# Kernel optimization log

Measured on AMD Instinct MI355X. Metric: run time of the kernel, lower is better.

The kernel has to match this reference:

```python
import jax, jax.numpy as jnp
import numpy as np

N_INP = 128
N_HID = 512
N_OUT = 256
N_HEADS = 64
N_SM = 4
EPS_GN = 1e-5
TINY = 1e-14


def setup_inputs() -> dict:
    key = jax.random.key(0)
    ks = jax.random.split(key, 8)
    s = 0.05  # small init scale keeps softplus/softmax in a sane range
    f32 = jnp.float32
    return {
        "x": jax.random.normal(ks[0], (N_INP, N_INP), f32),
        "last_out_sm": jax.random.uniform(ks[1], (N_OUT, N_HEADS), f32),
        # grouped-conv weights, stored per-head with conv singleton dims squeezed
        "qw": jax.random.normal(ks[2], (N_HEADS, N_INP), f32) * s,            # Conv2d q
        "w1": jax.random.normal(ks[3], (N_HEADS, N_HID, N_INP), f32) * s,     # Conv1d l1
        "gn1_g": jnp.ones((N_HEADS, N_HID), f32),                             # GroupNorm ln_l1
        "gn1_b": jnp.zeros((N_HEADS, N_HID), f32),
        "w2": jax.random.normal(ks[4], (N_SM, N_HEADS, N_OUT, N_HID), f32) * s,  # Conv1d l2_n
        "gn2_g": jnp.ones((N_SM, N_HEADS, N_OUT), f32),                       # GroupNorm ln_l2_n
        "gn2_b": jnp.zeros((N_SM, N_HEADS, N_OUT), f32),
        "ws": jax.random.normal(ks[5], (N_HEADS, N_OUT, N_OUT), f32) * s,     # Conv1d scalar
        "woo": jax.random.normal(ks[6], (N_HEADS, 2 * N_OUT), f32) * s,       # Conv1d on_off
    }


def _group_norm(z, g, b):
    # normalize over the last (per-head channel) axis, biased variance, then affine
    mu = z.mean(-1, keepdims=True)
    var = z.var(-1, keepdims=True)
    return (z - mu) * jax.lax.rsqrt(var + EPS_GN) * g + b


def reference(x, last_out_sm, qw, w1, gn1_g, gn1_b, w2, gn2_g, gn2_b, ws, woo):
    n_out = last_out_sm.shape[0]
    # q: grouped Conv2d with kernel (1, n_inp) on replicated x -> per-head x @ qw_h
    sub = jnp.einsum("rc,hc->hr", x, qw)                     # (H, n_inp)
    # l1 (grouped 1x1 conv == per-head matmul) + GroupNorm(n_heads groups) + softplus
    h1 = jax.nn.softplus(_group_norm(jnp.einsum("hoi,hi->ho", w1, sub), gn1_g, gn1_b))  # (H, n_hid)
    # l2_n branches: per-head matmul + GroupNorm + softmax over n_out, summed over n_sm
    z = _group_norm(jnp.einsum("shoi,hi->sho", w2, h1), gn2_g, gn2_b)  # (S, H, n_out)
    out_sm = jax.nn.softmax(z, axis=-1).sum(0).T             # (n_out, H)
    # scalar branch: grouped 1x1 conv applied to ones -> row-sum of per-head weight
    scalar = ws.sum(-1).T                                    # (n_out, H)
    # on_off gate: per-head dot of [prod(last_out_sm, dim1), out_sm[:, h]] with woo_h
    last_prod = jnp.prod(last_out_sm, axis=1)                # (n_out,)
    gate_logit = woo[:, :n_out] @ last_prod + jnp.einsum("ho,oh->h", woo[:, n_out:], out_sm)
    on_off = jax.nn.sigmoid(gate_logit)                      # (H,)
    on_off_out_sm = on_off[None, :] * out_sm                 # (n_out, H)
    out_scaled = on_off_out_sm * scalar
    out_scaled = jnp.where(jnp.abs(out_scaled) <= TINY, TINY, out_scaled)
    return (jnp.clip(on_off_out_sm, TINY, None), out_scaled)
```

## Files before the change

### kernel.cpp

```cpp
#include <hip/hip_runtime.h>
#include <math.h>

#define N_INP 128
#define N_HID 512
#define N_OUT 256
#define N_HEADS 64
#define N_SM 4
#define EPS_GN 1e-5f
#define TINY 1e-14f

__device__ __forceinline__ float wave_sum(float v) {
#pragma unroll
  for (int off = 32; off; off >>= 1) v += __shfl_down(v, off);
  return v;
}

__device__ __forceinline__ float block_sum(float v, float* red) {
  int wave = threadIdx.x >> 6, lane = threadIdx.x & 63;
  int nw = blockDim.x >> 6;
  v = wave_sum(v);
  __syncthreads();
  if (lane == 0) red[wave] = v;
  __syncthreads();
  float s = 0.f;
  for (int i = 0; i < nw; ++i) s += red[i];
  return s;
}

__global__ __launch_bounds__(512) void k_z1(
    const float* __restrict__ x, const float* __restrict__ qw,
    const float* __restrict__ w1, float* __restrict__ z1,
    float* __restrict__ zstat) {
  int blk = blockIdx.x;
  int h = blk >> 2, oq = blk & 3;
  int tid = threadIdx.x, wave = tid >> 6, lane = tid & 63;
  __shared__ float sub_s[N_INP];
  __shared__ float2 wred[8];

  float2 qv = ((const float2*)(qw + h * N_INP))[lane];
  for (int r = wave; r < N_INP; r += 8) {
    float2 xv = ((const float2*)(x + r * N_INP))[lane];
    float p = wave_sum(xv.x * qv.x + xv.y * qv.y);
    if (lane == 0) sub_s[r] = p;
  }
  __syncthreads();

  float2 sv = ((const float2*)sub_s)[lane];
  const float* w1h = w1 + ((size_t)h * N_HID + (size_t)oq * 128) * N_INP;
  float zs = 0.f, zq = 0.f;
  for (int k = 0; k < 16; ++k) {
    int o = wave * 16 + k;
    float2 wv = ((const float2*)(w1h + (size_t)o * N_INP))[lane];
    float p = wave_sum(wv.x * sv.x + wv.y * sv.y);
    if (lane == 0) { z1[h * N_HID + oq * 128 + o] = p; zs += p; zq += p * p; }
  }
  if (lane == 0) wred[wave] = make_float2(zs, zq);
  __syncthreads();
  if (tid == 0) {
    float a = 0.f, b = 0.f;
    for (int i = 0; i < 8; ++i) { a += wred[i].x; b += wred[i].y; }
    zstat[blk * 2] = a;
    zstat[blk * 2 + 1] = b;
  }
}

__global__ __launch_bounds__(1024) void k_l2(
    const float* __restrict__ z1, const float* __restrict__ zstat,
    const float* __restrict__ g1, const float* __restrict__ b1,
    const float* __restrict__ w2, const float* __restrict__ g2,
    const float* __restrict__ b2, const float* __restrict__ wsc,
    float* __restrict__ part, float* __restrict__ scal) {
  int blk = blockIdx.x;
  int s = blk >> 6, h = blk & 63;
  int tid = threadIdx.x, wave = tid >> 6, lane = tid & 63;
  __shared__ float h1_s[N_HID];
  __shared__ float z_s[N_OUT];
  __shared__ float2 red2[16];
  __shared__ float red[16];

  const float* w2base = w2 + (size_t)blk * N_OUT * N_HID;
  const float4* row0 = (const float4*)(w2base + (size_t)(wave * 16) * N_HID);
  float4 wa = row0[lane];
  float4 wb = row0[64 + lane];

  float zsum = 0.f, zsq = 0.f;
#pragma unroll
  for (int q = 0; q < 4; ++q) {
    zsum += zstat[(h * 4 + q) * 2];
    zsq  += zstat[(h * 4 + q) * 2 + 1];
  }
  float mu1 = zsum * (1.f / N_HID);
  float var1 = zsq * (1.f / N_HID) - mu1 * mu1;
  float r1 = rsqrtf(var1 + EPS_GN);
  if (tid < N_HID) {
    float v1 = z1[h * N_HID + tid];
    float zz = (v1 - mu1) * r1 * g1[h * N_HID + tid] + b1[h * N_HID + tid];
    h1_s[tid] = fmaxf(zz, 0.f) + log1pf(expf(-fabsf(zz)));
  }
  __syncthreads();

  float4 ha = ((const float4*)h1_s)[lane];
  float4 hb = ((const float4*)h1_s)[64 + lane];

  for (int k = 0; k < 4; ++k) {
    int o = s * 64 + wave * 4 + k;
    float4 v = ((const float4*)(wsc + ((size_t)(h * N_OUT + o)) * N_OUT))[lane];
    float p = wave_sum(v.x + v.y + v.z + v.w);
    if (lane == 0) scal[o * N_HEADS + h] = p;
  }

  float as = 0.f, aq = 0.f;
  for (int k = 0; k < 16; ++k) {
    float4 na, nb;
    if (k < 15) {
      const float4* row = (const float4*)(w2base + (size_t)(wave * 16 + k + 1) * N_HID);
      na = row[lane];
      nb = row[64 + lane];
    }
    float p = wa.x * ha.x + wa.y * ha.y + wa.z * ha.z + wa.w * ha.w +
              wb.x * hb.x + wb.y * hb.y + wb.z * hb.z + wb.w * hb.w;
    p = wave_sum(p);
    if (lane == 0) { z_s[wave * 16 + k] = p; as += p; aq += p * p; }
    wa = na; wb = nb;
  }
  if (lane == 0) red2[wave] = make_float2(as, aq);
  __syncthreads();

  float sx = 0.f, sy = 0.f;
  for (int i = 0; i < 16; ++i) { sx += red2[i].x; sy += red2[i].y; }
  float mu = sx * (1.f / N_OUT);
  float var = sy * (1.f / N_OUT) - mu * mu;
  float rs = rsqrtf(var + EPS_GN);
  float e = (tid < N_OUT)
                ? expf((z_s[tid] - mu) * rs * g2[(size_t)blk * N_OUT + tid] +
                       b2[(size_t)blk * N_OUT + tid])
                : 0.f;
  float es = block_sum(e, red);
  if (tid < N_OUT) part[(size_t)blk * N_OUT + tid] = e / es;
}

__global__ __launch_bounds__(256) void k_gate_final(
    const float* __restrict__ last, const float* __restrict__ woo,
    const float* __restrict__ part, const float* __restrict__ scal,
    float* __restrict__ out) {
  int h = blockIdx.x;
  int tid = threadIdx.x;
  __shared__ float red[4];

  float osum = 0.f;
#pragma unroll
  for (int ss = 0; ss < 4; ++ss)
    osum += part[(size_t)(ss * 64 + h) * N_OUT + tid];

  const float4* rowL = (const float4*)(last + (size_t)tid * N_HEADS);
  float lp = 1.f;
#pragma unroll
  for (int j = 0; j < 16; ++j) {
    float4 v = rowL[j];
    lp *= v.x * v.y * v.z * v.w;
  }
  float gpart = woo[h * 2 * N_OUT + tid] * lp +
                woo[h * 2 * N_OUT + N_OUT + tid] * osum;
  float logit = block_sum(gpart, red);
  float oo = 1.f / (1.f + expf(-logit));

  float v0 = oo * osum;
  out[tid * N_HEADS + h] = fmaxf(v0, TINY);
  float v1 = v0 * scal[tid * N_HEADS + h];
  out[N_OUT * N_HEADS + tid * N_HEADS + h] = (fabsf(v1) <= TINY) ? TINY : v1;
}

extern "C" void kernel_launch(void* const* d_in, const int* in_sizes, int n_in,
                              void* d_out, int out_size, void* d_ws, size_t ws_size,
                              hipStream_t stream) {
  const float* x    = (const float*)d_in[0];
  const float* last = (const float*)d_in[1];
  const float* qw   = (const float*)d_in[2];
  const float* w1   = (const float*)d_in[3];
  const float* g1   = (const float*)d_in[4];
  const float* b1   = (const float*)d_in[5];
  const float* w2   = (const float*)d_in[6];
  const float* g2   = (const float*)d_in[7];
  const float* b2   = (const float*)d_in[8];
  const float* wsc  = (const float*)d_in[9];
  const float* woo  = (const float*)d_in[10];
  float* out = (float*)d_out;
  float* ws  = (float*)d_ws;

  float* z1    = ws;
  float* zstat = ws + 32768;
  float* part  = ws + 33280;
  float* scal  = ws + 98816;

  hipLaunchKernelGGL(k_z1,        dim3(256), dim3(512),  0, stream,
                     x, qw, w1, z1, zstat);
  hipLaunchKernelGGL(k_l2,        dim3(256), dim3(1024), 0, stream,
                     z1, zstat, g1, b1, w2, g2, b2, wsc, part, scal);
  hipLaunchKernelGGL(k_gate_final,dim3(64),  dim3(256),  0, stream,
                     last, woo, part, scal, out);
}
```

Before: 256.0 us.

## Split waves into 16-lane groups for dot products to cut shuffle reductions

Result: faster. 243.4 us (-4.9%).

```diff
diff --git a/kernel.cpp b/kernel.cpp
--- a/kernel.cpp
+++ b/kernel.cpp
@@ -27,38 +27,59 @@
   return s;
 }
 
+__device__ __forceinline__ float group16_sum(float v) {
+#pragma unroll
+  for (int off = 8; off; off >>= 1) v += __shfl_down(v, off);
+  return v;
+}
+
 __global__ __launch_bounds__(512) void k_z1(
     const float* __restrict__ x, const float* __restrict__ qw,
     const float* __restrict__ w1, float* __restrict__ z1,
     float* __restrict__ zstat) {
   int blk = blockIdx.x;
   int h = blk >> 2, oq = blk & 3;
-  int tid = threadIdx.x, wave = tid >> 6, lane = tid & 63;
+  int tid = threadIdx.x, lane = tid & 63;
+  int g = lane >> 4, gl = lane & 15;
+  int grp = (tid >> 6) * 4 + g;
   __shared__ float sub_s[N_INP];
-  __shared__ float2 wred[8];
-
-  float2 qv = ((const float2*)(qw + h * N_INP))[lane];
-  for (int r = wave; r < N_INP; r += 8) {
-    float2 xv = ((const float2*)(x + r * N_INP))[lane];
-    float p = wave_sum(xv.x * qv.x + xv.y * qv.y);
-    if (lane == 0) sub_s[r] = p;
-  }
-  __syncthreads();
-
-  float2 sv = ((const float2*)sub_s)[lane];
+  __shared__ float2 wred[32];
+
+  const float4* qrow = (const float4*)(qw + (size_t)h * N_INP);
+  float4 Q0 = qrow[gl], Q1 = qrow[16 + gl];
+
+#pragma unroll
+  for (int j = 0; j < 4; ++j) {
+    int r = grp + 32 * j;
+    const float4* xr = (const float4*)(x + (size_t)r * N_INP);
+    float4 X0 = xr[gl], X1 = xr[16 + gl];
+    float p = X0.x * Q0.x + X0.y * Q0.y + X0.z * Q0.z + X0.w * Q0.w +
+              X1.x * Q1.x + X1.y * Q1.y + X1.z * Q1.z + X1.w * Q1.w;
+    p = group16_sum(p);
+    if (gl == 0) sub_s[r] = p;
+  }
+  __syncthreads();
+
+  const float4* sv = (const float4*)sub_s;
+  float4 S0 = sv[gl], S1 = sv[16 + gl];
   const float* w1h = w1 + ((size_t)h * N_HID + (size_t)oq * 128) * N_INP;
   float zs = 0.f, zq = 0.f;
-  for (int k = 0; k < 16; ++k) {
-    int o = wave * 16 + k;
-    float2 wv = ((const float2*)(w1h + (size_t)o * N_INP))[lane];
-    float p = wave_sum(wv.x * sv.x + wv.y * sv.y);
-    if (lane == 0) { z1[h * N_HID + oq * 128 + o] = p; zs += p; zq += p * p; }
-  }
-  if (lane == 0) wred[wave] = make_float2(zs, zq);
+#pragma unroll
+  for (int j = 0; j < 4; ++j) {
+    int o = grp + 32 * j;
+    const float4* wr = (const float4*)(w1h + (size_t)o * N_INP);
+    float4 W0 = wr[gl], W1 = wr[16 + gl];
+    float p = W0.x * S0.x + W0.y * S0.y + W0.z * S0.z + W0.w * S0.w +
+              W1.x * S1.x + W1.y * S1.y + W1.z * S1.z + W1.w * S1.w;
+    p = group16_sum(p);
+    if (gl == 0) { z1[h * N_HID + oq * 128 + o] = p; zs += p; zq += p * p; }
+  }
+  if (gl == 0) wred[grp] = make_float2(zs, zq);
   __syncthreads();
   if (tid == 0) {
     float a = 0.f, b = 0.f;
-    for (int i = 0; i < 8; ++i) { a += wred[i].x; b += wred[i].y; }
+#pragma unroll
+    for (int i = 0; i < 32; ++i) { a += wred[i].x; b += wred[i].y; }
     zstat[blk * 2] = a;
     zstat[blk * 2 + 1] = b;
   }
@@ -73,15 +94,21 @@
   int blk = blockIdx.x;
   int s = blk >> 6, h = blk & 63;
   int tid = threadIdx.x, wave = tid >> 6, lane = tid & 63;
+  int g = lane >> 4, gl = lane & 15;
   __shared__ float h1_s[N_HID];
   __shared__ float z_s[N_OUT];
-  __shared__ float2 red2[16];
+  __shared__ float2 red2[64];
   __shared__ float red[16];
 
   const float* w2base = w2 + (size_t)blk * N_OUT * N_HID;
-  const float4* row0 = (const float4*)(w2base + (size_t)(wave * 16) * N_HID);
-  float4 wa = row0[lane];
-  float4 wb = row0[64 + lane];
+  int row0 = wave * 16 + g;
+
+  float4 A[8], B[8];
+  {
+    const float4* rp = (const float4*)(w2base + (size_t)row0 * N_HID) + gl;
+#pragma unroll
+    for (int c = 0; c < 8; ++c) A[c] = rp[c * 16];
+  }
 
   float zsum = 0.f, zsq = 0.f;
 #pragma unroll
@@ -99,35 +126,47 @@
   }
   __syncthreads();
 
-  float4 ha = ((const float4*)h1_s)[lane];
-  float4 hb = ((const float4*)h1_s)[64 + lane];
-
-  for (int k = 0; k < 4; ++k) {
-    int o = s * 64 + wave * 4 + k;
-    float4 v = ((const float4*)(wsc + ((size_t)(h * N_OUT + o)) * N_OUT))[lane];
-    float p = wave_sum(v.x + v.y + v.z + v.w);
-    if (lane == 0) scal[o * N_HEADS + h] = p;
-  }
+  float4 H[8];
+#pragma unroll
+  for (int c = 0; c < 8; ++c) H[c] = ((const float4*)h1_s)[c * 16 + gl];
 
   float as = 0.f, aq = 0.f;
-  for (int k = 0; k < 16; ++k) {
-    float4 na, nb;
-    if (k < 15) {
-      const float4* row = (const float4*)(w2base + (size_t)(wave * 16 + k + 1) * N_HID);
-      na = row[lane];
-      nb = row[64 + lane];
+#pragma unroll
+  for (int r = 0; r < 4; ++r) {
+    if (r < 3) {
+      const float4* rp =
+          (const float4*)(w2base + (size_t)(row0 + (r + 1) * 4) * N_HID) + gl;
+#pragma unroll
+      for (int c = 0; c < 8; ++c) B[c] = rp[c * 16];
     }
-    float p = wa.x * ha.x + wa.y * ha.y + wa.z * ha.z + wa.w * ha.w +
-              wb.x * hb.x + wb.y * hb.y + wb.z * hb.z + wb.w * hb.w;
-    p = wave_sum(p);
-    if (lane == 0) { z_s[wave * 16 + k] = p; as += p; aq += p * p; }
-    wa = na; wb = nb;
-  }
-  if (lane == 0) red2[wave] = make_float2(as, aq);
+    float p = 0.f;
+#pragma unroll
+    for (int c = 0; c < 8; ++c)
+      p += A[c].x * H[c].x + A[c].y * H[c].y + A[c].z * H[c].z + A[c].w * H[c].w;
+    p = group16_sum(p);
+    if (gl == 0) {
+      z_s[row0 + r * 4] = p;
+      as += p; aq += p * p;
+    }
+#pragma unroll
+    for (int c = 0; c < 8; ++c) A[c] = B[c];
+  }
+  if (gl == 0) red2[wave * 4 + g] = make_float2(as, aq);
+
+  {
+    int o = s * 64 + wave * 4 + g;
+    const float4* wr = (const float4*)(wsc + ((size_t)h * N_OUT + o) * N_OUT) + gl;
+    float4 v0 = wr[0], v1 = wr[16], v2 = wr[32], v3 = wr[48];
+    float p = v0.x + v0.y + v0.z + v0.w + v1.x + v1.y + v1.z + v1.w +
+              v2.x + v2.y + v2.z + v2.w + v3.x + v3.y + v3.z + v3.w;
+    p = group16_sum(p);
+    if (gl == 0) scal[o * N_HEADS + h] = p;
+  }
   __syncthreads();
 
   float sx = 0.f, sy = 0.f;
-  for (int i = 0; i < 16; ++i) { sx += red2[i].x; sy += red2[i].y; }
+#pragma unroll
+  for (int i = 0; i < 64; ++i) { sx += red2[i].x; sy += red2[i].y; }
   float mu = sx * (1.f / N_OUT);
   float var = sy * (1.f / N_OUT) - mu * mu;
   float rs = rsqrtf(var + EPS_GN);
```
